# Kernel optimization log

Measured on AMD Instinct MI355X. Metric: run time of the kernel, lower is better.

## Reference

```python
import jax, jax.numpy as jnp
import numpy as np

B, S, D, H, DK, DFF = 4, 1024, 1024, 16, 64, 4096
EPS = 1e-5


def _layernorm(x, w, b):
    mu = jnp.mean(x, axis=-1, keepdims=True)
    var = jnp.mean((x - mu) ** 2, axis=-1, keepdims=True)
    return (x - mu) / jnp.sqrt(var + EPS) * w + b


def setup_inputs() -> dict:
    root = jax.random.key(0)
    ks = jax.random.split(root, 16)
    g = lambda k, shape, s=0.02: (jax.random.normal(k, shape, dtype=jnp.float32) * s)
    return {
        "mask": 1,
        "query": jax.random.normal(ks[0], (B, S, D), dtype=jnp.float32),
        "key": jax.random.normal(ks[1], (B, S, D), dtype=jnp.float32),
        "values": jax.random.normal(ks[2], (B, S, D), dtype=jnp.float32),
        "Wq": g(ks[3], (D, D)), "bq": jnp.zeros((D,), jnp.float32),
        "Wk": g(ks[4], (D, D)), "bk": jnp.zeros((D,), jnp.float32),
        "Wv": g(ks[5], (D, D)), "bv": jnp.zeros((D,), jnp.float32),
        "Wo": g(ks[6], (D, D)), "bo": jnp.zeros((D,), jnp.float32),
        "gammas": g(ks[7], (H, 1, 1), 0.5),
        "ln1_w": jnp.ones((D,), jnp.float32), "ln1_b": jnp.zeros((D,), jnp.float32),
        "W1": g(ks[8], (DFF, D)), "b1": jnp.zeros((DFF,), jnp.float32),
        "W2": g(ks[9], (D, DFF)), "b2": jnp.zeros((D,), jnp.float32),
        "ln2_w": jnp.ones((D,), jnp.float32), "ln2_b": jnp.zeros((D,), jnp.float32),
    }


def _forward(mask, query, key, values, Wq, bq, Wk, bk, Wv, bv, Wo, bo, gammas,
             ln1_w, ln1_b, W1, b1, W2, b2, ln2_w, ln2_b):
    # mask is a static Python int (the triu offset)
    allowed = jnp.triu(jnp.ones((S, S), dtype=jnp.float32), k=mask) == 0  # [S,S] bool

    def proj(x, W, b):  # [B,S,D] -> [B,H,S,DK]
        return (x @ W.T + b).reshape(B, S, H, DK).transpose(0, 2, 1, 3)

    q = proj(query, Wq, bq)
    k = proj(key, Wk, bk)
    v = proj(values, Wv, bv)

    scores = jnp.einsum('bhid,bhjd->bhij', q, k) / jnp.sqrt(jnp.float32(DK))

    # distance-decay factor, computed without gradient (torch.no_grad + detach)
    def dist_block(sc):
        sc_ = jax.nn.softmax(sc, axis=-1) * allowed.astype(sc.dtype)
        distcum = jnp.cumsum(sc_, axis=-1)
        disttot = jnp.sum(sc_, axis=-1, keepdims=True)
        idx = jnp.arange(S, dtype=jnp.float32)
        pos = jnp.abs(idx[None, :] - idx[:, None])[None, None]  # [1,1,S,S]
        return jnp.sqrt(jnp.clip((disttot - distcum) * pos, 0.0, None))
    dist_scores = jax.lax.stop_gradient(dist_block(scores))

    gamma = -jax.nn.softplus(gammas)[None]  # [1,H,1,1]
    total_effect = jnp.clip(jnp.exp(dist_scores * gamma), 1e-5, 1e5)
    scores = scores * total_effect
    scores = jnp.where(allowed, scores, jnp.float32(-1e20))
    attn = jax.nn.softmax(scores, axis=-1)
    if mask == 0:  # zero_pad first query row
        attn = attn.at[:, :, 0, :].set(0.0)

    out = jnp.einsum('bhij,bhjd->bhid', attn, v)
    concat = out.transpose(0, 2, 1, 3).reshape(B, S, D)
    attn_out = concat @ Wo.T + bo

    x = _layernorm(query + attn_out, ln1_w, ln1_b)
    ffn = jax.nn.relu(x @ W1.T + b1) @ W2.T + b2
    return _layernorm(x + ffn, ln2_w, ln2_b)


def reference(mask, query, key, values, Wq, bq, Wk, bk, Wv, bv, Wo, bo, gammas,
              ln1_w, ln1_b, W1, b1, W2, b2, ln2_w, ln2_b):
    return _forward(mask, query, key, values, Wq, bq, Wk, bk, Wv, bv, Wo, bo,
                    gammas, ln1_w, ln1_b, W1, b1, W2, b2, ln2_w, ln2_b)
```

## Files before the change

kernel.cpp:

```cpp
#include <hip/hip_runtime.h>
#include <hip/hip_bf16.h>
#include <math.h>

#define BB   4
#define SS   1024
#define DDIM 1024
#define HH   16
#define DKK  64
#define DFFF 4096
#define JC2  64

typedef __attribute__((ext_vector_type(8))) short short8;
typedef __attribute__((ext_vector_type(4))) float f32x4;
typedef unsigned short ushort;

__device__ __forceinline__ ushort f2bf(float f) {
    unsigned int u = __float_as_uint(f);
    unsigned int r = (u + 0x7FFFu + ((u >> 16) & 1u)) >> 16;
    return (ushort)r;
}
__device__ __forceinline__ short8 pack8(float4 f0, float4 f1) {
    short8 s;
    s[0] = (short)f2bf(f0.x); s[1] = (short)f2bf(f0.y);
    s[2] = (short)f2bf(f0.z); s[3] = (short)f2bf(f0.w);
    s[4] = (short)f2bf(f1.x); s[5] = (short)f2bf(f1.y);
    s[6] = (short)f2bf(f1.z); s[7] = (short)f2bf(f1.w);
    return s;
}

#define GLD16(g, l) __builtin_amdgcn_global_load_lds( \
    (const __attribute__((address_space(1))) unsigned int*)(g), \
    (__attribute__((address_space(3))) unsigned int*)(l), 16, 0, 0)

__device__ __forceinline__ float fexp2(float x) { return __builtin_amdgcn_exp2f(x); }

__device__ __forceinline__ float scan16(float x) {
    x += __int_as_float(__builtin_amdgcn_update_dpp(0, __float_as_int(x), 0x111, 0xF, 0xF, true));
    x += __int_as_float(__builtin_amdgcn_update_dpp(0, __float_as_int(x), 0x112, 0xF, 0xF, true));
    x += __int_as_float(__builtin_amdgcn_update_dpp(0, __float_as_int(x), 0x114, 0xF, 0xF, true));
    x += __int_as_float(__builtin_amdgcn_update_dpp(0, __float_as_int(x), 0x118, 0xF, 0xF, true));
    return x;
}
__device__ __forceinline__ float bcast15(float x) {
    return __int_as_float(__builtin_amdgcn_ds_swizzle(__float_as_int(x), 0x1F0));
}

__device__ __forceinline__ float block_reduce_sum(float v, float* red, int tid) {
#pragma unroll
    for (int off = 32; off; off >>= 1) v += __shfl_xor(v, off);
    __syncthreads();
    if ((tid & 63) == 0) red[tid >> 6] = v;
    __syncthreads();
    return red[0] + red[1] + red[2] + red[3];
}

struct CvtArgs { const float* s[6]; ushort* d[6]; unsigned int n[6]; };
__global__ __launch_bounds__(256) void convert_bf(CvtArgs a) {
    const int seg = blockIdx.y;
    size_t idx = ((size_t)blockIdx.x * 256 + threadIdx.x) * 8;
    if (idx >= a.n[seg]) return;
    const float* s = a.s[seg];
    float4 f0 = *(const float4*)(s + idx);
    float4 f1 = *(const float4*)(s + idx + 4);
    *(short8*)(a.d[seg] + idx) = pack8(f0, f1);
}

template <int BM, typename TC, bool RELU, bool BIAS, bool CVTA>
__device__ __forceinline__ void gemm_core(const void* __restrict__ Av, int lda,
                                          const ushort* __restrict__ Bm, int ldb,
                                          const float* __restrict__ bias,
                                          TC* __restrict__ C, int N, int Klen,
                                          int bm, int bn) {
    constexpr int MT = BM / 32;
    constexpr int PA = BM / 32;
    __shared__ ushort A_s[BM * 64];
    __shared__ ushort B_s[128 * 64];
    const int t = threadIdx.x;
    const int lane = t & 63, w = t >> 6;
    const int wr = w >> 1, wc = w & 1;
    const int fm = lane & 15, fq = lane >> 4;
    const int srl = lane >> 3;
    const int sg8 = ((lane & 7) ^ srl) << 3;

    f32x4 acc[MT][4];
#pragma unroll
    for (int mt = 0; mt < MT; mt++)
#pragma unroll
        for (int nt = 0; nt < 4; nt++) acc[mt][nt] = (f32x4){0.f, 0.f, 0.f, 0.f};

    for (int kt = 0; kt < Klen; kt += 64) {
        __syncthreads();
        if constexpr (CVTA) {
            const float* Af = (const float*)Av;
#pragma unroll
            for (int p = 0; p < PA; ++p) {
                int rowg = (w * PA + p) * 8;
                const float* src = Af + (size_t)(bm + rowg + srl) * lda + kt + sg8;
                float4 f0 = *(const float4*)(src);
                float4 f1 = *(const float4*)(src + 4);
                *(short8*)&A_s[(rowg + srl) * 64 + ((lane & 7) << 3)] = pack8(f0, f1);
            }
        } else {
            const ushort* A = (const ushort*)Av;
#pragma unroll
            for (int p = 0; p < PA; ++p) {
                int rowg = (w * PA + p) * 8;
                GLD16(A + (size_t)(bm + rowg + srl) * lda + kt + sg8, &A_s[rowg * 64]);
            }
        }
#pragma unroll
        for (int p = 0; p < 4; ++p) {
            int rowg = (w * 4 + p) * 8;
            GLD16(Bm + (size_t)(bn + rowg + srl) * ldb + kt + sg8, &B_s[rowg * 64]);
        }
        __syncthreads();

        short8 av[2][MT], bv[2][4];
        const int sw = fm & 7;
#pragma unroll
        for (int mt = 0; mt < MT; ++mt) {
            int row = wr * (BM / 2) + mt * 16 + fm;
#pragma unroll
            for (int ks = 0; ks < 2; ++ks)
                av[ks][mt] = *(const short8*)&A_s[row * 64 + (((ks * 4 + fq) ^ sw) << 3)];
        }
#pragma unroll
        for (int nt = 0; nt < 4; ++nt) {
            int row = wc * 64 + nt * 16 + fm;
#pragma unroll
            for (int ks = 0; ks < 2; ++ks)
                bv[ks][nt] = *(const short8*)&B_s[row * 64 + (((ks * 4 + fq) ^ sw) << 3)];
        }
#pragma unroll
        for (int ks = 0; ks < 2; ++ks)
#pragma unroll
            for (int mt = 0; mt < MT; ++mt)
#pragma unroll
                for (int nt = 0; nt < 4; ++nt)
                    acc[mt][nt] = __builtin_amdgcn_mfma_f32_16x16x32_bf16(
                        av[ks][mt], bv[ks][nt], acc[mt][nt], 0, 0, 0);
    }

#pragma unroll
    for (int mt = 0; mt < MT; mt++) {
        int row0 = bm + wr * (BM / 2) + mt * 16 + fq * 4;
#pragma unroll
        for (int nt = 0; nt < 4; nt++) {
            int col = bn + wc * 64 + nt * 16 + fm;
            float bsv = BIAS ? bias[col] : 0.f;
#pragma unroll
            for (int r = 0; r < 4; r++) {
                float val = acc[mt][nt][r] + bsv;
                if (RELU) val = fmaxf(val, 0.f);
                if constexpr (sizeof(TC) == 4)
                    ((float*)C)[(size_t)(row0 + r) * N + col] = val;
                else
                    ((ushort*)C)[(size_t)(row0 + r) * N + col] = f2bf(val);
            }
        }
    }
}

template <int BM, typename TC, bool RELU>
__global__ __launch_bounds__(256, 2) void gemm_bf(const ushort* __restrict__ A,
                                                  const ushort* __restrict__ Bm,
                                                  const float* __restrict__ bias,
                                                  TC* __restrict__ C,
                                                  int N, int K) {
    gemm_core<BM, TC, RELU, true, false>(A, K, Bm, K, bias, C, N, K,
                                         blockIdx.y * BM, blockIdx.x * 128);
}

struct QkvArgs { const float* A[3]; const ushort* B[3]; const float* bias[3]; ushort* C[3]; };
__global__ __launch_bounds__(256, 2) void gemm_qkv(QkvArgs qa) {
    const int g = blockIdx.z;
    gemm_core<128, ushort, false, true, true>(qa.A[g], DDIM, qa.B[g], DDIM,
                                              qa.bias[g], qa.C[g], DDIM, DDIM,
                                              blockIdx.y * 128, blockIdx.x * 128);
}

struct SkArgs { const ushort* A; const ushort* Bm; float* C0; float* C1; int lda; int Klen; };
__global__ __launch_bounds__(256, 2) void gemm_splitk(SkArgs s) {
    const int z = blockIdx.z;
    float* C = z ? s.C1 : s.C0;
    const int koff = z * s.Klen;
    gemm_core<128, float, false, false, false>(s.A + koff, s.lda, s.Bm + koff, s.lda,
                                               nullptr, C, DDIM, s.Klen,
                                               blockIdx.y * 128, blockIdx.x * 128);
}

__global__ __launch_bounds__(256, 4) void attn_flash(
    const ushort* __restrict__ Q, const ushort* __restrict__ Kg,
    const ushort* __restrict__ Vg, const float* __restrict__ gammas,
    const int* __restrict__ maskp, ushort* __restrict__ out) {
    __shared__ short QP[64 * 72];
    __shared__ short KsD[2][64 * 64];
    __shared__ short Vts[64 * 72];

    const int t = threadIdx.x;
    const int lane = t & 63, w = t >> 6;
    const int col = lane & 15;
    const int quad = lane >> 4;
    const int srl = lane >> 3;
    const int sg8 = ((lane & 7) ^ srl) << 3;
    const int swk = col & 7;

    const int bid = blockIdx.x;
    const int xcls = bid & 7;
    const int m = bid >> 3;
    const int bh = xcls + ((m & 7) << 3);
    const int itr = m >> 3;
    const int yy = itr & 3, jj = itr >> 2;
    const int it = (((yy + jj) & 3) << 2) + ((2 * yy + jj) & 3);
    const int h = bh & (HH - 1);
    const int b = bh >> 4;
    const int i0 = it * 64;
    const int mask = *maskp;

    const float LOG2E = 1.44269504f;
    const float SC2 = 0.125f * LOG2E;
    const float g0 = gammas[h];
    const float gnat = -((g0 > 20.f) ? g0 : log1pf(__expf(g0)));
    const float g2 = gnat * LOG2E;

    const size_t qbase = ((size_t)(b * SS + i0)) * DDIM + h * DKK;
    const size_t kvbase = ((size_t)b * SS) * DDIM + h * DKK;

#define STAGE_K(jc, kb) \
    { _Pragma("unroll") for (int p = 0; p < 2; ++p) { \
        int rowg = (w * 2 + p) * 8; \
        GLD16(Kg + kvbase + (size_t)((jc) + rowg + srl) * DDIM + sg8, \
              &KsD[kb][rowg * 64]); } }

    {
        int r = t >> 2, d0 = (t & 3) << 4;
        const ushort* gq = Q + qbase + (size_t)r * DDIM + d0;
        *(short8*)&QP[r * 72 + d0]     = *(const short8*)(gq);
        *(short8*)&QP[r * 72 + d0 + 8] = *(const short8*)(gq + 8);
        STAGE_K(0, 0);
    }
    __syncthreads();
    const short8 qa0 = *(const short8*)&QP[(w * 16 + col) * 72 + quad * 8];
    const short8 qa1 = *(const short8*)&QP[(w * 16 + col) * 72 + 32 + quad * 8];

    float m1[4], su[4], smT[4], gi4[4];
    int lim4[4];
#pragma unroll
    for (int r = 0; r < 4; ++r) {
        m1[r] = -3.4e38f; su[r] = 0.f; smT[r] = 0.f;
        int gi = i0 + w * 16 + quad * 4 + r;
        gi4[r] = (float)gi;
        lim4[r] = gi + mask;
    }

    int buf = 0;
    for (int ck = 0; ck < SS / JC2; ++ck) {
        const int jc = ck * JC2;
        const int njc = ((ck + 1) & 15) * JC2;
        STAGE_K(njc, buf ^ 1);
#pragma unroll
        for (int g = 0; g < 4; ++g) {
            const short* Kr = &KsD[buf][(g * 16 + col) * 64];
            short8 kb0 = *(const short8*)&Kr[(quad ^ swk) << 3];
            short8 kb1 = *(const short8*)&Kr[((4 + quad) ^ swk) << 3];
            f32x4 c = (f32x4){0.f, 0.f, 0.f, 0.f};
            c = __builtin_amdgcn_mfma_f32_16x16x32_bf16(qa0, kb0, c, 0, 0, 0);
            c = __builtin_amdgcn_mfma_f32_16x16x32_bf16(qa1, kb1, c, 0, 0, 0);
            int j = jc + g * 16 + col;
#pragma unroll
            for (int r = 0; r < 4; ++r) {
                float s2 = c[r] * SC2;
                m1[r] = fmaxf(m1[r], s2);
                float ev = fexp2(s2);
                su[r] += ev;
                smT[r] += (j < lim4[r]) ? ev : 0.f;
            }
        }
        __syncthreads();
        buf ^= 1;
    }
#pragma unroll
    for (int off = 1; off < 16; off <<= 1) {
#pragma unroll
        for (int r = 0; r < 4; ++r) {
            m1[r] = fmaxf(m1[r], __shfl_xor(m1[r], off, 16));
            su[r] += __shfl_xor(su[r], off, 16);
            smT[r] += __shfl_xor(smT[r], off, 16);
        }
    }
    float lse2[4], smTn[4], ms2[4];
#pragma unroll
    for (int r = 0; r < 4; ++r) {
        lse2[r] = __log2f(su[r]);
        smTn[r] = smT[r] / su[r];
        ms2[r]  = fmaxf(m1[r], 0.f);
    }

    const int nck2 = min(SS / JC2, max(1, (i0 + 62 + mask) / 64 + 1));

    float l2[4], carry[4];
    f32x4 o[4];
#pragma unroll
    for (int r = 0; r < 4; ++r) { l2[r] = 0.f; carry[r] = 0.f; }
#pragma unroll
    for (int dg = 0; dg < 4; ++dg) o[dg] = (f32x4){0.f, 0.f, 0.f, 0.f};

    short* Pw = &QP[w * 16 * 72];

    for (int ck = 0; ck < nck2; ++ck) {
        const int jc = ck * JC2;
        if (ck + 1 < nck2) STAGE_K((ck + 1) * JC2, buf ^ 1);
        {
            int j = t & 63, dq = t >> 6, d0 = dq * 16;
            const ushort* gv = Vg + kvbase + (size_t)(jc + j) * DDIM + d0;
            short8 v0 = *(const short8*)(gv);
            short8 v1 = *(const short8*)(gv + 8);
#pragma unroll
            for (int k = 0; k < 8; ++k) {
                Vts[(d0 + k) * 72 + j]     = v0[k];
                Vts[(d0 + 8 + k) * 72 + j] = v1[k];
            }
        }

#pragma unroll
        for (int g = 0; g < 4; ++g) {
            const short* Kr = &KsD[buf][(g * 16 + col) * 64];
            short8 kb0 = *(const short8*)&Kr[(quad ^ swk) << 3];
            short8 kb1 = *(const short8*)&Kr[((4 + quad) ^ swk) << 3];
            f32x4 c = (f32x4){0.f, 0.f, 0.f, 0.f};
            c = __builtin_amdgcn_mfma_f32_16x16x32_bf16(qa0, kb0, c, 0, 0, 0);
            c = __builtin_amdgcn_mfma_f32_16x16x32_bf16(qa1, kb1, c, 0, 0, 0);
            const int j = jc + g * 16 + col;
            const float jf = (float)j;
#pragma unroll
            for (int r = 0; r < 4; ++r) {
                float s2 = c[r] * SC2;
                float pj = fexp2(s2 - lse2[r]);
                float incl = (j < lim4[r]) ? pj : 0.f;
                incl = scan16(incl);
                float tot = bcast15(incl);
                float Cc = carry[r] + incl;
                carry[r] += tot;
                float pos = fabsf(jf - gi4[r]);
                float d2 = fmaxf((smTn[r] - Cc) * pos, 0.f);
                float dist = __builtin_amdgcn_sqrtf(d2);
                float eff = fmaxf(fexp2(g2 * dist), 1e-5f);
                float pe = fexp2(s2 * eff - ms2[r]);
                float p = (j < lim4[r]) ? pe : 0.f;
                l2[r] += p;
                Pw[(quad * 4 + r) * 72 + g * 16 + col] = (short)f2bf(p);
            }
        }
        __syncthreads();
#pragma unroll
        for (int kg = 0; kg < 2; ++kg) {
            short8 pa = *(const short8*)&Pw[col * 72 + kg * 32 + quad * 8];
#pragma unroll
            for (int dg = 0; dg < 4; ++dg) {
                short8 vb = *(const short8*)&Vts[(dg * 16 + col) * 72 + kg * 32 + quad * 8];
                o[dg] = __builtin_amdgcn_mfma_f32_16x16x32_bf16(pa, vb, o[dg], 0, 0, 0);
            }
        }
        __syncthreads();
        buf ^= 1;
    }

#pragma unroll
    for (int off = 1; off < 16; off <<= 1)
#pragma unroll
        for (int r = 0; r < 4; ++r) l2[r] += __shfl_xor(l2[r], off, 16);

#pragma unroll
    for (int r = 0; r < 4; ++r) {
        int irow = i0 + w * 16 + quad * 4 + r;
        float scl = 1.f / l2[r];
        if (mask == 0 && irow == 0) scl = 0.f;
        size_t base = ((size_t)(b * SS) + irow) * DDIM + h * DKK;
#pragma unroll
        for (int dg = 0; dg < 4; ++dg)
            out[base + dg * 16 + col] = f2bf(o[dg][r] * scl);
    }
#undef STAGE_K
}

template <bool WB>
__global__ __launch_bounds__(256) void add_ln(const float* __restrict__ R,
                                              const float* __restrict__ Y0,
                                              const float* __restrict__ Y1,
                                              const float* __restrict__ gb,
                                              const float* __restrict__ w,
                                              const float* __restrict__ bb,
                                              float* __restrict__ out,
                                              ushort* __restrict__ obf) {
    const int row = blockIdx.x;
    const int tid = threadIdx.x;
    __shared__ float red[4];
    __shared__ float xs[DDIM];
    const size_t base = (size_t)row * DDIM;
    float s = 0.f, s2 = 0.f;
#pragma unroll
    for (int l = 0; l < 4; l++) {
        int idx = tid + l * 256;
        float x = R[base + idx] + Y0[base + idx] + Y1[base + idx] + gb[idx];
        xs[idx] = x;
        s += x;
        s2 += x * x;
    }
    s = block_reduce_sum(s, red, tid);
    s2 = block_reduce_sum(s2, red, tid);
    const float mu = s * (1.f / DDIM);
    const float var = s2 * (1.f / DDIM) - mu * mu;
    const float rstd = rsqrtf(var + 1e-5f);
#pragma unroll
    for (int l = 0; l < 4; l++) {
        int idx = tid + l * 256;
        float v = (xs[idx] - mu) * rstd * w[idx] + bb[idx];
        out[base + idx] = v;
        if (WB) obf[base + idx] = f2bf(v);
    }
}

extern "C" void kernel_launch(void* const* d_in, const int* in_sizes, int n_in,
                              void* d_out, int out_size, void* d_ws, size_t ws_size,
                              hipStream_t stream) {
    const int*   maskp  = (const int*)d_in[0];
    const float* query  = (const float*)d_in[1];
    const float* key    = (const float*)d_in[2];
    const float* values = (const float*)d_in[3];
    const float* Wq = (const float*)d_in[4];
    const float* bq = (const float*)d_in[5];
    const float* Wk = (const float*)d_in[6];
    const float* bk = (const float*)d_in[7];
    const float* Wv = (const float*)d_in[8];
    const float* bv = (const float*)d_in[9];
    const float* Wo = (const float*)d_in[10];
    const float* bo = (const float*)d_in[11];
    const float* gammas = (const float*)d_in[12];
    const float* ln1w = (const float*)d_in[13];
    const float* ln1b = (const float*)d_in[14];
    const float* W1 = (const float*)d_in[15];
    const float* b1 = (const float*)d_in[16];
    const float* W2 = (const float*)d_in[17];
    const float* b2 = (const float*)d_in[18];
    const float* ln2w = (const float*)d_in[19];
    const float* ln2b = (const float*)d_in[20];

    const int M = BB * SS;
    const size_t MB = 1048576;
    char* wsb = (char*)d_ws;
    ushort* Wq_bf = (ushort*)(wsb + 0 * MB);
    ushort* Wk_bf = (ushort*)(wsb + 8 * MB);
    ushort* Wv_bf = (ushort*)(wsb + 16 * MB);
    ushort* Wo_bf = (ushort*)(wsb + 24 * MB);
    ushort* W1_bf = (ushort*)(wsb + 32 * MB);
    ushort* W2_bf = (ushort*)(wsb + 40 * MB);
    ushort* Qb    = (ushort*)(wsb + 72 * MB);
    ushort* Kb    = (ushort*)(wsb + 80 * MB);
    ushort* Vb    = (ushort*)(wsb + 88 * MB);
    ushort* ATTb  = (ushort*)(wsb + 96 * MB);
    float*  Ysp0  = (float*)(wsb + 104 * MB);
    float*  Ysp1  = (float*)(wsb + 120 * MB);
    float*  xf    = (float*)(wsb + 48 * MB);
    ushort* x_bf  = (ushort*)(wsb + 64 * MB);
    ushort* hidden= (ushort*)(wsb + 72 * MB);

    dim3 blk(256);

    const unsigned int N4M = 4u * 1024 * 1024, N1M = 1024 * 1024;
    CvtArgs ca;
    ca.s[0] = Wq; ca.s[1] = Wk; ca.s[2] = Wv; ca.s[3] = Wo;
    ca.s[4] = W1; ca.s[5] = W2;
    ca.d[0] = Wq_bf; ca.d[1] = Wk_bf; ca.d[2] = Wv_bf; ca.d[3] = Wo_bf;
    ca.d[4] = W1_bf; ca.d[5] = W2_bf;
    ca.n[0] = N1M; ca.n[1] = N1M; ca.n[2] = N1M; ca.n[3] = N1M;
    ca.n[4] = N4M; ca.n[5] = N4M;
    convert_bf<<<dim3(2048, 6), blk, 0, stream>>>(ca);

    QkvArgs qa;
    qa.A[0] = query; qa.A[1] = key; qa.A[2] = values;
    qa.B[0] = Wq_bf; qa.B[1] = Wk_bf; qa.B[2] = Wv_bf;
    qa.bias[0] = bq; qa.bias[1] = bk; qa.bias[2] = bv;
    qa.C[0] = Qb; qa.C[1] = Kb; qa.C[2] = Vb;
    gemm_qkv<<<dim3(8, 32, 3), blk, 0, stream>>>(qa);

    attn_flash<<<dim3(BB * HH * 16), blk, 0, stream>>>(Qb, Kb, Vb, gammas, maskp, ATTb);

    {
        SkArgs s; s.A = ATTb; s.Bm = Wo_bf; s.C0 = Ysp0; s.C1 = Ysp1;
        s.lda = DDIM; s.Klen = DDIM / 2;
        gemm_splitk<<<dim3(8, 32, 2), blk, 0, stream>>>(s);
    }

    add_ln<true><<<dim3(M), blk, 0, stream>>>(query, Ysp0, Ysp1, bo, ln1w, ln1b, xf, x_bf);

    gemm_bf<128, ushort, true><<<dim3(32, 32), blk, 0, stream>>>(x_bf, W1_bf, b1, hidden, DFFF, DDIM);

    {
        SkArgs s; s.A = hidden; s.Bm = W2_bf; s.C0 = Ysp0; s.C1 = Ysp1;
        s.lda = DFFF; s.Klen = DFFF / 2;
        gemm_splitk<<<dim3(8, 32, 2), blk, 0, stream>>>(s);
    }

    add_ln<false><<<dim3(M), blk, 0, stream>>>(xf, Ysp0, Ysp1, b2, ln2w, ln2b, (float*)d_out, nullptr);
}
```

Baseline: 400.7 us.

## Replace W1 FFN GEMM with 256x256-tile 8-wave phased pipelined kernel

Swaps the 128x128-tile 256-thread GEMM used for the first FFN projection for a new 512-thread kernel with 256x256 tiles and double-buffered LDS. Each k-step is split into four phases that interleave global-to-LDS prefetch of the next tile with MFMA work, using explicit vmcnt waits, barriers and priority raises. The goal is more data reuse per tile and better overlap of memory loads with matrix math. In exchange it needs 128KB of LDS per block and many accumulator registers, and the grid shrinks to 16x16 blocks, which lowers occupancy and may leave CUs idle.

New measurement: 404.9 us. No clear change (+1.0%).

```diff
diff --git a/kernel.cpp b/kernel.cpp
--- a/kernel.cpp
+++ b/kernel.cpp
@@ -161,16 +161,6 @@
     }
 }
 
-template <int BM, typename TC, bool RELU>
-__global__ __launch_bounds__(256, 2) void gemm_bf(const ushort* __restrict__ A,
-                                                  const ushort* __restrict__ Bm,
-                                                  const float* __restrict__ bias,
-                                                  TC* __restrict__ C,
-                                                  int N, int K) {
-    gemm_core<BM, TC, RELU, true, false>(A, K, Bm, K, bias, C, N, K,
-                                         blockIdx.y * BM, blockIdx.x * 128);
-}
-
 struct QkvArgs { const float* A[3]; const ushort* B[3]; const float* bias[3]; ushort* C[3]; };
 __global__ __launch_bounds__(256, 2) void gemm_qkv(QkvArgs qa) {
     const int g = blockIdx.z;
@@ -187,6 +177,143 @@
     gemm_core<128, float, false, false, false>(s.A + koff, s.lda, s.Bm + koff, s.lda,
                                                nullptr, C, DDIM, s.Klen,
                                                blockIdx.y * 128, blockIdx.x * 128);
+}
+
+template <typename TC, bool RELU, bool BIAS>
+__global__ __launch_bounds__(512, 2) void gemm_8ph(const ushort* __restrict__ A,
+                                                   const ushort* __restrict__ Bm,
+                                                   const float* __restrict__ bias,
+                                                   TC* __restrict__ C,
+                                                   int N, int K) {
+    __shared__ ushort Asb[2][256 * 64];
+    __shared__ ushort Bsb[2][256 * 64];
+    const int t = threadIdx.x;
+    const int lane = t & 63, w = t >> 6;
+    const int wr = w >> 2, wc = w & 3;
+    const int fm = lane & 15, fq = lane >> 4;
+    const int swr = fm & 7;
+    const int hh = t >> 8;
+    const int sg8 = ((t & 7) ^ ((t >> 3) & 7)) << 3;
+    const int bm = blockIdx.y * 256, bn = blockIdx.x * 256;
+
+#define STB(i, dbuf, kt) GLD16(Bm + (size_t)(bn + (i) * 64 + (t >> 3)) * K + (kt) + sg8, \
+                               &Bsb[dbuf][((i) * 64 + w * 8) * 64])
+#define STA(s, dbuf, kt) GLD16(A + (size_t)(bm + hh * 128 + (s) * 32 + (w & 3) * 8 + (lane >> 3)) * K + (kt) + sg8, \
+                               &Asb[dbuf][(hh * 128 + (s) * 32 + (w & 3) * 8) * 64])
+#define PH_END(NVM) \
+    asm volatile("s_waitcnt vmcnt(" #NVM ")" ::: "memory"); \
+    __builtin_amdgcn_s_barrier(); \
+    __builtin_amdgcn_sched_barrier(0);
+
+    f32x4 acc[8][4];
+#pragma unroll
+    for (int mi = 0; mi < 8; ++mi)
+#pragma unroll
+        for (int n = 0; n < 4; ++n) acc[mi][n] = (f32x4){0.f, 0.f, 0.f, 0.f};
+
+    STB(0, 0, 0); STB(1, 0, 0); STB(2, 0, 0); STB(3, 0, 0);
+    STA(0, 0, 0); STA(1, 0, 0); STA(2, 0, 0); STA(3, 0, 0);
+    PH_END(3)
+
+    int c = 0;
+    short8 av[2][2], bv[4][2];
+    for (int kt = 0; kt < K; kt += 64) {
+        const int nkt = kt + 64;
+        const bool pf = nkt < K;
+        const int cn = c ^ 1;
+#pragma unroll
+        for (int n = 0; n < 4; ++n)
+#pragma unroll
+            for (int ks = 0; ks < 2; ++ks)
+                bv[n][ks] = *(const short8*)&Bsb[c][(wc * 64 + n * 16 + fm) * 64 + (((ks * 4 + fq) ^ swr) << 3)];
+#pragma unroll
+        for (int ml = 0; ml < 2; ++ml)
+#pragma unroll
+            for (int ks = 0; ks < 2; ++ks)
+                av[ml][ks] = *(const short8*)&Asb[c][(wr * 128 + ml * 16 + fm) * 64 + (((ks * 4 + fq) ^ swr) << 3)];
+        if (pf) { STB(0, cn, nkt); STB(1, cn, nkt); STB(2, cn, nkt); }
+        __builtin_amdgcn_s_setprio(1);
+#pragma unroll
+        for (int ks = 0; ks < 2; ++ks)
+#pragma unroll
+            for (int ml = 0; ml < 2; ++ml)
+#pragma unroll
+                for (int n = 0; n < 4; ++n)
+                    acc[ml][n] = __builtin_amdgcn_mfma_f32_16x16x32_bf16(av[ml][ks], bv[n][ks], acc[ml][n], 0, 0, 0);
+        __builtin_amdgcn_s_setprio(0);
+        PH_END(5)
+#pragma unroll
+        for (int ml = 0; ml < 2; ++ml)
+#pragma unroll
+            for (int ks = 0; ks < 2; ++ks)
+                av[ml][ks] = *(const short8*)&Asb[c][(wr * 128 + (2 + ml) * 16 + fm) * 64 + (((ks * 4 + fq) ^ swr) << 3)];
+        if (pf) { STB(3, cn, nkt); STA(0, cn, nkt); }
+        __builtin_amdgcn_s_setprio(1);
+#pragma unroll
+        for (int ks = 0; ks < 2; ++ks)
+#pragma unroll
+            for (int ml = 0; ml < 2; ++ml)
+#pragma unroll
+                for (int n = 0; n < 4; ++n)
+                    acc[2 + ml][n] = __builtin_amdgcn_mfma_f32_16x16x32_bf16(av[ml][ks], bv[n][ks], acc[2 + ml][n], 0, 0, 0);
+        __builtin_amdgcn_s_setprio(0);
+        PH_END(6)
+#pragma unroll
+        for (int ml = 0; ml < 2; ++ml)
+#pragma unroll
+            for (int ks = 0; ks < 2; ++ks)
+                av[ml][ks] = *(const short8*)&Asb[c][(wr * 128 + (4 + ml) * 16 + fm) * 64 + (((ks * 4 + fq) ^ swr) << 3)];
+        if (pf) { STA(1, cn, nkt); STA(2, cn, nkt); }
+        __builtin_amdgcn_s_setprio(1);
+#pragma unroll
+        for (int ks = 0; ks < 2; ++ks)
+#pragma unroll
+            for (int ml = 0; ml < 2; ++ml)
+#pragma unroll
+                for (int n = 0; n < 4; ++n)
+                    acc[4 + ml][n] = __builtin_amdgcn_mfma_f32_16x16x32_bf16(av[ml][ks], bv[n][ks], acc[4 + ml][n], 0, 0, 0);
+        __builtin_amdgcn_s_setprio(0);
+        PH_END(7)
+#pragma unroll
+        for (int ml = 0; ml < 2; ++ml)
+#pragma unroll
+            for (int ks = 0; ks < 2; ++ks)
+                av[ml][ks] = *(const short8*)&Asb[c][(wr * 128 + (6 + ml) * 16 + fm) * 64 + (((ks * 4 + fq) ^ swr) << 3)];
+        if (pf) { STA(3, cn, nkt); }
+        __builtin_amdgcn_s_setprio(1);
+#pragma unroll
+        for (int ks = 0; ks < 2; ++ks)
+#pragma unroll
+            for (int ml = 0; ml < 2; ++ml)
+#pragma unroll
+                for (int n = 0; n < 4; ++n)
+                    acc[6 + ml][n] = __builtin_amdgcn_mfma_f32_16x16x32_bf16(av[ml][ks], bv[n][ks], acc[6 + ml][n], 0, 0, 0);
+        __builtin_amdgcn_s_setprio(0);
+        PH_END(3)
+        c = cn;
+    }
+
+#pragma unroll
+    for (int mi = 0; mi < 8; ++mi) {
+        int row0 = bm + wr * 128 + mi * 16 + fq * 4;
+#pragma unroll
+        for (int n = 0; n < 4; ++n) {
+            int col = bn + wc * 64 + n * 16 + fm;
+            float bsv = BIAS ? bias[col] : 0.f;
+#pragma unroll
+            for (int r = 0; r < 4; ++r) {
+                float val = acc[mi][n][r] + bsv;
+                if (RELU) val = fmaxf(val, 0.f);
+                if constexpr (sizeof(TC) == 4)
+                    ((float*)C)[(size_t)(row0 + r) * N + col] = val;
+                else
+                    ((ushort*)C)[(size_t)(row0 + r) * N + col] = f2bf(val);
+            }
+        }
+    }
+#undef STB
+#undef STA
+#undef PH_END
 }
 
 __global__ __launch_bounds__(256, 4) void attn_flash(
@@ -493,7 +620,8 @@
 
     add_ln<true><<<dim3(M), blk, 0, stream>>>(query, Ysp0, Ysp1, bo, ln1w, ln1b, xf, x_bf);
 
-    gemm_bf<128, ushort, true><<<dim3(32, 32), blk, 0, stream>>>(x_bf, W1_bf, b1, hidden, DFFF, DDIM);
+    gemm_8ph<ushort, true, true><<<dim3(DFFF / 256, M / 256), dim3(512), 0, stream>>>(
+        x_bf, W1_bf, b1, hidden, DFFF, DDIM);
 
     {
         SkArgs s; s.A = hidden; s.Bm = W2_bf; s.C0 = Ysp0; s.C1 = Ysp1;
```
